# Optimization experiments

Hardware: AMD Instinct MI355X
Metric: run time of the kernel (lower is better)

The kernel has to match this reference:

```python
import jax, jax.numpy as jnp
import numpy as np

BANDWIDTH = 0.001
THRESHOLD_INIT = 0.01


def setup_inputs() -> dict:
    key = jax.random.key(0)
    k1, k2, k3 = jax.random.split(key, 3)
    N, d_model, d_sae = 8192, 2048, 16384
    x = jax.random.normal(k1, (N, d_model), dtype=jnp.float32)
    # scale ~ 1/sqrt(d) so pre-activations are O(1) and threshold=0.01 gives sparsity
    W_enc = jax.random.normal(k2, (d_model, d_sae), dtype=jnp.float32) / np.sqrt(d_model)
    b_enc = jnp.zeros((d_sae,), dtype=jnp.float32)
    threshold = jnp.full((d_sae,), THRESHOLD_INIT, dtype=jnp.float32)
    W_dec = jax.random.normal(k3, (d_sae, d_model), dtype=jnp.float32) / np.sqrt(d_sae)
    b_dec = jnp.zeros((d_model,), dtype=jnp.float32)
    return {"x": x, "W_enc": W_enc, "b_enc": b_enc, "threshold": threshold,
            "W_dec": W_dec, "b_dec": b_dec}


def reference(x, W_enc, b_enc, threshold, W_dec, b_dec):
    # encode: F.linear(x - b_dec, W_enc.t(), b_enc) == (x - b_dec) @ W_enc + b_enc
    pre = (x - b_dec) @ W_enc + b_enc                      # [N, d_sae]
    mask = (pre > threshold).astype(pre.dtype)
    features = pre * mask                                   # JumpReLU
    # decode: features @ W_dec + b_dec
    reconstruction = features @ W_dec + b_dec               # [N, d_model]
    return (reconstruction, features)
```

## Files before the change

kernel.cpp:

```cpp
#include <hip/hip_runtime.h>
#include <hip/hip_bf16.h>


typedef __bf16 bf16x8 __attribute__((ext_vector_type(8)));
typedef float  f32x4  __attribute__((ext_vector_type(4)));

__device__ __forceinline__ short f2bf(float f) {
    unsigned u = __float_as_uint(f);
    unsigned r = u + 0x7FFF + ((u >> 16) & 1);
    return (short)(r >> 16);
}

__device__ __forceinline__ void gl_lds16(const void* g, void* l) {
    __builtin_amdgcn_global_load_lds(
        (const __attribute__((address_space(1))) unsigned int*)g,
        (__attribute__((address_space(3))) unsigned int*)l, 16, 0, 0);
}

__device__ __forceinline__ void fence_bar() {
    asm volatile("" ::: "memory");
    __builtin_amdgcn_s_barrier();
    asm volatile("" ::: "memory");
}

__global__ __launch_bounds__(256) void prep_x(const float* __restrict__ x,
                                              const float* __restrict__ b_dec,
                                              short* __restrict__ xb) {
    int idx = (blockIdx.x * 256 + threadIdx.x) * 4;
    float4 v = *(const float4*)(x + idx);
    int k = idx & 2047;
    float4 b = *(const float4*)(b_dec + k);
    short4 o;
    o.x = f2bf(v.x - b.x);
    o.y = f2bf(v.y - b.y);
    o.z = f2bf(v.z - b.z);
    o.w = f2bf(v.w - b.w);
    *(short4*)(xb + idx) = o;
}

__global__ __launch_bounds__(256) void transpose_cvt64(const float* __restrict__ in,
                                                       short* __restrict__ out,
                                                       int R, int C) {
    __shared__ short t[32][66];
    const int tid = threadIdx.x;
    const int c0 = blockIdx.x * 32;
    const int r0 = blockIdx.y * 64;
#pragma unroll
    for (int i = 0; i < 8; ++i) {
        int idx = tid + i * 256;
        int r = idx >> 5, c = idx & 31;
        t[c][r] = f2bf(in[(size_t)(r0 + r) * C + (c0 + c)]);
    }
    __syncthreads();
#pragma unroll
    for (int i = 0; i < 4; ++i) {
        int idx = tid + i * 256;
        int orow = idx >> 5, chunk = idx & 31;
        *(short2*)(&out[(size_t)(c0 + orow) * R + r0 + chunk * 2]) =
            *(const short2*)(&t[orow][chunk * 2]);
    }
}

__global__ __launch_bounds__(512, 1) void gemm256(
    const short* __restrict__ A, const short* __restrict__ Bt,
    const float* __restrict__ bias, const float* __restrict__ thr,
    float* __restrict__ Cf, short* __restrict__ Cb,
    int M, int N, int K) {
    __shared__ short As[2][256 * 64];
    __shared__ short Bs[2][256 * 64];

    const int tid  = threadIdx.x;
    const int lane = tid & 63;
    const int wave = tid >> 6;
    const int wm   = wave >> 2;
    const int wn   = wave & 3;

    const int Mt   = M >> 8;
    const int nwg  = gridDim.x * gridDim.y;
    const int orig = blockIdx.y * gridDim.x + blockIdx.x;
    const int wg   = (orig & 7) * (nwg >> 3) + (orig >> 3);
    const int bm   = wg % Mt;
    const int bn   = wg / Mt;

    const short* Abase = A  + (size_t)bm * 256 * K;
    const short* Bbase = Bt + (size_t)bn * 256 * K;

    const int srow = tid >> 3;
    const int csel = ((((tid & 7) << 4) ^ ((srow & 7) << 4)) >> 1);

    const int mrow = lane & 15;
    const int hi16 = (lane >> 4) << 4;
    const int swz  = (mrow & 7) << 4;

    f32x4 acc[8][4];
#pragma unroll
    for (int i = 0; i < 8; ++i)
#pragma unroll
        for (int j = 0; j < 4; ++j)
            acc[i][j] = (f32x4){0.f, 0.f, 0.f, 0.f};

    auto stage = [&](int buf, int h, int t) {
        const short* gb = ((h < 2) ? Abase : Bbase)
                          + (size_t)((h & 1) * 128 + srow) * K + t * 64 + csel;
        char* lb = (char*)((h < 2) ? As[buf] : Bs[buf]) + (h & 1) * 16384 + wave * 1024;
        gl_lds16(gb, lb);
        gl_lds16(gb + (size_t)64 * K, lb + 8192);
    };

    const int NT = K >> 6;

    stage(0, 0, 0); stage(0, 1, 0); stage(0, 2, 0); stage(0, 3, 0);
    stage(1, 0, 1);
    asm volatile("s_waitcnt vmcnt(2)" ::: "memory");
    fence_bar();

    bf16x8 af[4][2], bq[2][2];

    for (int t = 0; t < NT; ++t) {
        const int cur = t & 1, nxt = cur ^ 1;
        const char* Ard = (const char*)As[cur] + (wm * 128 + mrow) * 128;
        const char* Brd = (const char*)Bs[cur] + (wn * 64 + mrow) * 128;

#pragma unroll
        for (int mi = 0; mi < 4; ++mi)
#pragma unroll
            for (int kk = 0; kk < 2; ++kk)
                af[mi][kk] = *(const bf16x8*)(Ard + mi * 2048 + ((kk * 64 + hi16) ^ swz));
#pragma unroll
        for (int ni = 0; ni < 2; ++ni)
#pragma unroll
            for (int kk = 0; kk < 2; ++kk)
                bq[ni][kk] = *(const bf16x8*)(Brd + ni * 2048 + ((kk * 64 + hi16) ^ swz));
        if (t + 1 < NT) stage(nxt, 1, t + 1);
        fence_bar();
        asm volatile("s_waitcnt lgkmcnt(0)" ::: "memory");
        __builtin_amdgcn_s_setprio(1);
#pragma unroll
        for (int mi = 0; mi < 4; ++mi)
#pragma unroll
            for (int ni = 0; ni < 2; ++ni)
#pragma unroll
                for (int kk = 0; kk < 2; ++kk)
                    acc[mi][ni] = __builtin_amdgcn_mfma_f32_16x16x32_bf16(
                        af[mi][kk], bq[ni][kk], acc[mi][ni], 0, 0, 0);
        __builtin_amdgcn_s_setprio(0);
        fence_bar();

#pragma unroll
        for (int ni = 0; ni < 2; ++ni)
#pragma unroll
            for (int kk = 0; kk < 2; ++kk)
                bq[ni][kk] = *(const bf16x8*)(Brd + (2 + ni) * 2048 + ((kk * 64 + hi16) ^ swz));
        if (t + 1 < NT) stage(nxt, 2, t + 1);
        fence_bar();
        asm volatile("s_waitcnt lgkmcnt(0)" ::: "memory");
        __builtin_amdgcn_s_setprio(1);
#pragma unroll
        for (int mi = 0; mi < 4; ++mi)
#pragma unroll
            for (int ni = 0; ni < 2; ++ni)
#pragma unroll
                for (int kk = 0; kk < 2; ++kk)
                    acc[mi][2 + ni] = __builtin_amdgcn_mfma_f32_16x16x32_bf16(
                        af[mi][kk], bq[ni][kk], acc[mi][2 + ni], 0, 0, 0);
        __builtin_amdgcn_s_setprio(0);
        fence_bar();

#pragma unroll
        for (int mi = 0; mi < 4; ++mi)
#pragma unroll
            for (int kk = 0; kk < 2; ++kk)
                af[mi][kk] = *(const bf16x8*)(Ard + (4 + mi) * 2048 + ((kk * 64 + hi16) ^ swz));
        if (t + 1 < NT) stage(nxt, 3, t + 1);
        fence_bar();
        asm volatile("s_waitcnt lgkmcnt(0)" ::: "memory");
        __builtin_amdgcn_s_setprio(1);
#pragma unroll
        for (int mi = 0; mi < 4; ++mi)
#pragma unroll
            for (int ni = 0; ni < 2; ++ni)
#pragma unroll
                for (int kk = 0; kk < 2; ++kk)
                    acc[4 + mi][2 + ni] = __builtin_amdgcn_mfma_f32_16x16x32_bf16(
                        af[mi][kk], bq[ni][kk], acc[4 + mi][2 + ni], 0, 0, 0);
        __builtin_amdgcn_s_setprio(0);
        fence_bar();

#pragma unroll
        for (int ni = 0; ni < 2; ++ni)
#pragma unroll
            for (int kk = 0; kk < 2; ++kk)
                bq[ni][kk] = *(const bf16x8*)(Brd + ni * 2048 + ((kk * 64 + hi16) ^ swz));
        if (t + 2 < NT) stage(cur, 0, t + 2);
        fence_bar();
        asm volatile("s_waitcnt lgkmcnt(0)" ::: "memory");
        __builtin_amdgcn_s_setprio(1);
#pragma unroll
        for (int mi = 0; mi < 4; ++mi)
#pragma unroll
            for (int ni = 0; ni < 2; ++ni)
#pragma unroll
                for (int kk = 0; kk < 2; ++kk)
                    acc[4 + mi][ni] = __builtin_amdgcn_mfma_f32_16x16x32_bf16(
                        af[mi][kk], bq[ni][kk], acc[4 + mi][ni], 0, 0, 0);
        __builtin_amdgcn_s_setprio(0);
        if (t + 2 < NT) {
            asm volatile("s_waitcnt vmcnt(2)" ::: "memory");
        } else if (t + 1 < NT) {
            asm volatile("s_waitcnt vmcnt(0)" ::: "memory");
        }
        fence_bar();
    }

    const int colb = bn * 256 + wn * 64 + mrow;
    const int rowb = bm * 256 + wm * 128 + ((lane >> 4) << 2);
    float bz[4], tz[4];
#pragma unroll
    for (int ni = 0; ni < 4; ++ni) {
        bz[ni] = bias[colb + ni * 16];
        tz[ni] = thr ? thr[colb + ni * 16] : 0.f;
    }
#pragma unroll
    for (int mi = 0; mi < 8; ++mi) {
#pragma unroll
        for (int ni = 0; ni < 4; ++ni) {
#pragma unroll
            for (int r = 0; r < 4; ++r) {
                float v = acc[mi][ni][r] + bz[ni];
                if (thr) v = (v > tz[ni]) ? v : 0.f;
                size_t off = (size_t)(rowb + mi * 16 + r) * N + colb + ni * 16;
                Cf[off] = v;
                if (Cb) Cb[off] = f2bf(v);
            }
        }
    }
}

extern "C" void kernel_launch(void* const* d_in, const int* in_sizes, int n_in,
                              void* d_out, int out_size, void* d_ws, size_t ws_size,
                              hipStream_t stream) {
    const float* x      = (const float*)d_in[0];
    const float* W_enc  = (const float*)d_in[1];
    const float* b_enc  = (const float*)d_in[2];
    const float* thr    = (const float*)d_in[3];
    const float* W_dec  = (const float*)d_in[4];
    const float* b_dec  = (const float*)d_in[5];

    const int N = 8192, DM = 2048, DS = 16384;

    float* recon = (float*)d_out;
    float* feats = (float*)d_out + (size_t)N * DM;

    char* ws = (char*)d_ws;
    short* xb    = (short*)ws;
    short* wencT = (short*)(ws + ((size_t)32 << 20));
    short* wdecT = (short*)(ws + ((size_t)96 << 20));
    short* fb    = (short*)(ws + ((size_t)160 << 20));

    prep_x<<<(N * DM) / (256 * 4), 256, 0, stream>>>(x, b_dec, xb);
    transpose_cvt64<<<dim3(DS / 32, DM / 64), 256, 0, stream>>>(W_enc, wencT, DM, DS);
    transpose_cvt64<<<dim3(DM / 32, DS / 64), 256, 0, stream>>>(W_dec, wdecT, DS, DM);

    gemm256<<<dim3(N / 256, DS / 256), 512, 0, stream>>>(
        xb, wencT, b_enc, thr, feats, fb, N, DS, DM);
    gemm256<<<dim3(N / 256, DM / 256), 512, 0, stream>>>(
        fb, wdecT, b_dec, nullptr, recon, nullptr, N, DM, DS);
}
```

Measured before the change: 2.342 ms.

## Restructure GEMM prefetch schedule with split B fragments and fewer barriers

The GEMM main loop now holds the low and high B fragments in separate registers, which lets the last MFMA phase reuse the already-loaded low fragment instead of reloading it. Staging is reordered so the two B halves of the next-next tile are issued two iterations ahead, with vmcnt raised to 4. Several barriers and lgkmcnt waits between phases are removed to cut synchronisation stalls. The weight transpose kernel also moves to 128-row tiles with 8-byte stores; the new schedule adds register pressure and correctness depends on the changed wait counts and buffer reuse ordering.

```diff
diff --git a/kernel.cpp b/kernel.cpp
--- a/kernel.cpp
+++ b/kernel.cpp
@@ -38,15 +38,15 @@
     *(short4*)(xb + idx) = o;
 }
 
-__global__ __launch_bounds__(256) void transpose_cvt64(const float* __restrict__ in,
-                                                       short* __restrict__ out,
-                                                       int R, int C) {
-    __shared__ short t[32][66];
+__global__ __launch_bounds__(256) void transpose_cvt128(const float* __restrict__ in,
+                                                        short* __restrict__ out,
+                                                        int R, int C) {
+    __shared__ short t[32][130];
     const int tid = threadIdx.x;
     const int c0 = blockIdx.x * 32;
-    const int r0 = blockIdx.y * 64;
-#pragma unroll
-    for (int i = 0; i < 8; ++i) {
+    const int r0 = blockIdx.y * 128;
+#pragma unroll
+    for (int i = 0; i < 16; ++i) {
         int idx = tid + i * 256;
         int r = idx >> 5, c = idx & 31;
         t[c][r] = f2bf(in[(size_t)(r0 + r) * C + (c0 + c)]);
@@ -55,9 +55,13 @@
 #pragma unroll
     for (int i = 0; i < 4; ++i) {
         int idx = tid + i * 256;
-        int orow = idx >> 5, chunk = idx & 31;
-        *(short2*)(&out[(size_t)(c0 + orow) * R + r0 + chunk * 2]) =
-            *(const short2*)(&t[orow][chunk * 2]);
+        int oc = idx >> 5, rc = idx & 31;
+        short4 v;
+        v.x = t[oc][rc * 4 + 0];
+        v.y = t[oc][rc * 4 + 1];
+        v.z = t[oc][rc * 4 + 2];
+        v.w = t[oc][rc * 4 + 3];
+        *(short4*)(&out[(size_t)(c0 + oc) * R + r0 + rc * 4]) = v;
     }
 }
 
@@ -110,11 +114,11 @@
     const int NT = K >> 6;
 
     stage(0, 0, 0); stage(0, 1, 0); stage(0, 2, 0); stage(0, 3, 0);
-    stage(1, 0, 1);
-    asm volatile("s_waitcnt vmcnt(2)" ::: "memory");
+    stage(1, 2, 1); stage(1, 3, 1);
+    asm volatile("s_waitcnt vmcnt(4)" ::: "memory");
     fence_bar();
 
-    bf16x8 af[4][2], bq[2][2];
+    bf16x8 af[4][2], bqlo[2][2], bqhi[2][2];
 
     for (int t = 0; t < NT; ++t) {
         const int cur = t & 1, nxt = cur ^ 1;
@@ -130,30 +134,26 @@
         for (int ni = 0; ni < 2; ++ni)
 #pragma unroll
             for (int kk = 0; kk < 2; ++kk)
-                bq[ni][kk] = *(const bf16x8*)(Brd + ni * 2048 + ((kk * 64 + hi16) ^ swz));
+                bqlo[ni][kk] = *(const bf16x8*)(Brd + ni * 2048 + ((kk * 64 + hi16) ^ swz));
+        if (t + 1 < NT) stage(nxt, 0, t + 1);
+        __builtin_amdgcn_s_setprio(1);
+#pragma unroll
+        for (int mi = 0; mi < 4; ++mi)
+#pragma unroll
+            for (int ni = 0; ni < 2; ++ni)
+#pragma unroll
+                for (int kk = 0; kk < 2; ++kk)
+                    acc[mi][ni] = __builtin_amdgcn_mfma_f32_16x16x32_bf16(
+                        af[mi][kk], bqlo[ni][kk], acc[mi][ni], 0, 0, 0);
+        __builtin_amdgcn_s_setprio(0);
+        fence_bar();
+
+#pragma unroll
+        for (int ni = 0; ni < 2; ++ni)
+#pragma unroll
+            for (int kk = 0; kk < 2; ++kk)
+                bqhi[ni][kk] = *(const bf16x8*)(Brd + (2 + ni) * 2048 + ((kk * 64 + hi16) ^ swz));
         if (t + 1 < NT) stage(nxt, 1, t + 1);
-        fence_bar();
-        asm volatile("s_waitcnt lgkmcnt(0)" ::: "memory");
-        __builtin_amdgcn_s_setprio(1);
-#pragma unroll
-        for (int mi = 0; mi < 4; ++mi)
-#pragma unroll
-            for (int ni = 0; ni < 2; ++ni)
-#pragma unroll
-                for (int kk = 0; kk < 2; ++kk)
-                    acc[mi][ni] = __builtin_amdgcn_mfma_f32_16x16x32_bf16(
-                        af[mi][kk], bq[ni][kk], acc[mi][ni], 0, 0, 0);
-        __builtin_amdgcn_s_setprio(0);
-        fence_bar();
-
-#pragma unroll
-        for (int ni = 0; ni < 2; ++ni)
-#pragma unroll
-            for (int kk = 0; kk < 2; ++kk)
-                bq[ni][kk] = *(const bf16x8*)(Brd + (2 + ni) * 2048 + ((kk * 64 + hi16) ^ swz));
-        if (t + 1 < NT) stage(nxt, 2, t + 1);
-        fence_bar();
-        asm volatile("s_waitcnt lgkmcnt(0)" ::: "memory");
         __builtin_amdgcn_s_setprio(1);
 #pragma unroll
         for (int mi = 0; mi < 4; ++mi)
@@ -162,7 +162,7 @@
 #pragma unroll
                 for (int kk = 0; kk < 2; ++kk)
                     acc[mi][2 + ni] = __builtin_amdgcn_mfma_f32_16x16x32_bf16(
-                        af[mi][kk], bq[ni][kk], acc[mi][2 + ni], 0, 0, 0);
+                        af[mi][kk], bqhi[ni][kk], acc[mi][2 + ni], 0, 0, 0);
         __builtin_amdgcn_s_setprio(0);
         fence_bar();
 
@@ -171,9 +171,7 @@
 #pragma unroll
             for (int kk = 0; kk < 2; ++kk)
                 af[mi][kk] = *(const bf16x8*)(Ard + (4 + mi) * 2048 + ((kk * 64 + hi16) ^ swz));
-        if (t + 1 < NT) stage(nxt, 3, t + 1);
-        fence_bar();
-        asm volatile("s_waitcnt lgkmcnt(0)" ::: "memory");
+        if (t + 2 < NT) stage(cur, 2, t + 2);
         __builtin_amdgcn_s_setprio(1);
 #pragma unroll
         for (int mi = 0; mi < 4; ++mi)
@@ -182,18 +180,11 @@
 #pragma unroll
                 for (int kk = 0; kk < 2; ++kk)
                     acc[4 + mi][2 + ni] = __builtin_amdgcn_mfma_f32_16x16x32_bf16(
-                        af[mi][kk], bq[ni][kk], acc[4 + mi][2 + ni], 0, 0, 0);
-        __builtin_amdgcn_s_setprio(0);
-        fence_bar();
-
-#pragma unroll
-        for (int ni = 0; ni < 2; ++ni)
-#pragma unroll
-            for (int kk = 0; kk < 2; ++kk)
-                bq[ni][kk] = *(const bf16x8*)(Brd + ni * 2048 + ((kk * 64 + hi16) ^ swz));
-        if (t + 2 < NT) stage(cur, 0, t + 2);
-        fence_bar();
-        asm volatile("s_waitcnt lgkmcnt(0)" ::: "memory");
+                        af[mi][kk], bqhi[ni][kk], acc[4 + mi][2 + ni], 0, 0, 0);
+        __builtin_amdgcn_s_setprio(0);
+        fence_bar();
+
+        if (t + 2 < NT) stage(cur, 3, t + 2);
         __builtin_amdgcn_s_setprio(1);
 #pragma unroll
         for (int mi = 0; mi < 4; ++mi)
@@ -202,10 +193,10 @@
 #pragma unroll
                 for (int kk = 0; kk < 2; ++kk)
                     acc[4 + mi][ni] = __builtin_amdgcn_mfma_f32_16x16x32_bf16(
-                        af[mi][kk], bq[ni][kk], acc[4 + mi][ni], 0, 0, 0);
+                        af[mi][kk], bqlo[ni][kk], acc[4 + mi][ni], 0, 0, 0);
         __builtin_amdgcn_s_setprio(0);
         if (t + 2 < NT) {
-            asm volatile("s_waitcnt vmcnt(2)" ::: "memory");
+            asm volatile("s_waitcnt vmcnt(4)" ::: "memory");
         } else if (t + 1 < NT) {
             asm volatile("s_waitcnt vmcnt(0)" ::: "memory");
         }
@@ -258,8 +249,8 @@
     short* fb    = (short*)(ws + ((size_t)160 << 20));
 
     prep_x<<<(N * DM) / (256 * 4), 256, 0, stream>>>(x, b_dec, xb);
-    transpose_cvt64<<<dim3(DS / 32, DM / 64), 256, 0, stream>>>(W_enc, wencT, DM, DS);
-    transpose_cvt64<<<dim3(DM / 32, DS / 64), 256, 0, stream>>>(W_dec, wdecT, DS, DM);
+    transpose_cvt128<<<dim3(DS / 32, DM / 128), 256, 0, stream>>>(W_enc, wencT, DM, DS);
+    transpose_cvt128<<<dim3(DM / 32, DS / 128), 256, 0, stream>>>(W_dec, wdecT, DS, DM);
 
     gemm256<<<dim3(N / 256, DS / 256), 512, 0, stream>>>(
         xb, wencT, b_enc, thr, feats, fb, N, DS, DM);
```

Result: faster. 2.221 ms (-5.2%).
